# Kernel optimization log

Measured on AMD Instinct MI355X. Metric: run time of the kernel, lower is better.

Reference implementation:

```python
import jax, jax.numpy as jnp
import numpy as np

K = 3  # spatial kernel size (TVConv_k_square == 9)


def setup_inputs() -> dict:
    key = jax.random.key(0)
    k1, k2 = jax.random.split(key)
    B, C, H, W = 8, 96, 128, 128
    x = jax.random.normal(k1, (B, C, H, W), dtype=jnp.float32)
    weight_maps = jax.random.normal(k2, (1, C, K, K, H, W), dtype=jnp.float32)
    return {"x": x, "weight_maps": weight_maps}


def reference(x, weight_maps):
    # Per-pixel spatially-varying 3x3 depthwise conv.
    B, C, H, W = x.shape
    xp = jnp.pad(x, ((0, 0), (0, 0), (1, 1), (1, 1)))  # zero pad, (B,C,H+2,W+2)
    # Gather the 9 shifted views (equivalent to the as_strided unfold, stride 1).
    patches = jnp.stack(
        [xp[:, :, i:i + H, j:j + W] for i in range(K) for j in range(K)], axis=2
    ).reshape(B, C, K, K, H, W)
    # Weighted sum over the 3x3 window per channel per pixel.
    out = (weight_maps * patches).sum(axis=(2, 3))  # (B,C,H,W)
    return out
```

## Files before the change

### kernel.cpp

```cpp
#include <hip/hip_runtime.h>


namespace {
constexpr int B = 8, C = 96, H = 128, W = 128;
constexpr int HW = H * W;
}

__global__ __launch_bounds__(256, 6) void tvconv_kernel(
    const float* __restrict__ x,
    const float* __restrict__ wm,
    float* __restrict__ out) {
  const int t  = threadIdx.x;
  const int c  = blockIdx.x >> 4;
  const int h0 = (blockIdx.x & 15) * 8;
  const int lr = t >> 5;
  const int w4 = t & 31;
  const int h  = h0 + lr;
  const int w  = w4 * 4;

  const float4 zero4 = make_float4(0.f, 0.f, 0.f, 0.f);

  const float* wp = wm + (size_t)c * 9 * HW + h * W + w;
  float4 wt[9];
#pragma unroll
  for (int k = 0; k < 9; ++k) {
    wt[k] = *reinterpret_cast<const float4*>(wp + (size_t)k * HW);
  }

  if (h == 0)     { wt[0] = zero4; wt[1] = zero4; wt[2] = zero4; }
  if (h == H - 1) { wt[6] = zero4; wt[7] = zero4; wt[8] = zero4; }
  const int up = (h == 0)     ? 0 : W;
  const int dn = (h == H - 1) ? 0 : W;

  const bool at_left  = (w4 == 0);
  const bool at_right = (w4 == 31);

  const float* xb = x   + (size_t)c * HW + h * W + w;
  float*       ob = out + (size_t)c * HW + h * W + w;

#pragma unroll
  for (int b = 0; b < B; ++b) {
    const float4 r0 = *reinterpret_cast<const float4*>(xb - up);
    const float4 r1 = *reinterpret_cast<const float4*>(xb);
    const float4 r2 = *reinterpret_cast<const float4*>(xb + dn);
    const float4 rows[3] = {r0, r1, r2};

    float acc[4] = {0.f, 0.f, 0.f, 0.f};
#pragma unroll
    for (int i = 0; i < 3; ++i) {
      const float4 ctr = rows[i];
      float left  = __shfl_up(ctr.w, 1);
      float right = __shfl_down(ctr.x, 1);
      if (at_left)  left  = 0.f;
      if (at_right) right = 0.f;
      const float xv[6] = {left, ctr.x, ctr.y, ctr.z, ctr.w, right};
#pragma unroll
      for (int j = 0; j < 3; ++j) {
        const float4 wv = wt[i * 3 + j];
        const float wa[4] = {wv.x, wv.y, wv.z, wv.w};
#pragma unroll
        for (int m = 0; m < 4; ++m) {
          acc[m] += wa[m] * xv[m + j];
        }
      }
    }
    float4 o;
    o.x = acc[0]; o.y = acc[1]; o.z = acc[2]; o.w = acc[3];
    *reinterpret_cast<float4*>(ob) = o;

    xb += (size_t)C * HW;
    ob += (size_t)C * HW;
  }
}

extern "C" void kernel_launch(void* const* d_in, const int* in_sizes, int n_in,
                              void* d_out, int out_size, void* d_ws, size_t ws_size,
                              hipStream_t stream) {
  const float* x  = (const float*)d_in[0];
  const float* wm = (const float*)d_in[1];
  float* out = (float*)d_out;

  const int blocks = C * (H / 8);
  tvconv_kernel<<<blocks, 256, 0, stream>>>(x, wm, out);
}
```

Measured before the change: 140.9 us.

## Share row loads across wave halves via cross-lane shuffle, prefetch next batch, nontemporal I/O

Each thread now loads only its own row and one neighbour row, and gets the third row from the partner half-wave with __shfl_xor(…,32), cutting input loads per batch from three to two. Loads for the next batch are issued before the current one is computed, to hide memory latency. Weight-map loads and output stores use nontemporal hints to keep them out of the cache. The trade-off is extra shuffles, more live registers, and the possibility that the nontemporal hints lower cache reuse of the weights.

```diff
diff --git a/kernel.cpp b/kernel.cpp
--- a/kernel.cpp
+++ b/kernel.cpp
@@ -5,6 +5,8 @@
 constexpr int B = 8, C = 96, H = 128, W = 128;
 constexpr int HW = H * W;
 }
+
+typedef float f4 __attribute__((ext_vector_type(4)));
 
 __global__ __launch_bounds__(256, 6) void tvconv_kernel(
     const float* __restrict__ x,
@@ -18,19 +20,21 @@
   const int h  = h0 + lr;
   const int w  = w4 * 4;
 
-  const float4 zero4 = make_float4(0.f, 0.f, 0.f, 0.f);
-
   const float* wp = wm + (size_t)c * 9 * HW + h * W + w;
-  float4 wt[9];
+  f4 wt[9];
 #pragma unroll
   for (int k = 0; k < 9; ++k) {
-    wt[k] = *reinterpret_cast<const float4*>(wp + (size_t)k * HW);
+    wt[k] = __builtin_nontemporal_load(
+        reinterpret_cast<const f4*>(wp + (size_t)k * HW));
   }
 
-  if (h == 0)     { wt[0] = zero4; wt[1] = zero4; wt[2] = zero4; }
-  if (h == H - 1) { wt[6] = zero4; wt[7] = zero4; wt[8] = zero4; }
+  if (h == 0)     { wt[0] = 0.f; wt[1] = 0.f; wt[2] = 0.f; }
+  if (h == H - 1) { wt[6] = 0.f; wt[7] = 0.f; wt[8] = 0.f; }
   const int up = (h == 0)     ? 0 : W;
   const int dn = (h == H - 1) ? 0 : W;
+
+  const bool lower = ((lr & 1) == 0);
+  const int ooff = lower ? -up : dn;
 
   const bool at_left  = (w4 == 0);
   const bool at_right = (w4 == 31);
@@ -38,17 +42,34 @@
   const float* xb = x   + (size_t)c * HW + h * W + w;
   float*       ob = out + (size_t)c * HW + h * W + w;
 
+  f4 nctr = *reinterpret_cast<const f4*>(xb);
+  f4 noth = *reinterpret_cast<const f4*>(xb + ooff);
+
 #pragma unroll
   for (int b = 0; b < B; ++b) {
-    const float4 r0 = *reinterpret_cast<const float4*>(xb - up);
-    const float4 r1 = *reinterpret_cast<const float4*>(xb);
-    const float4 r2 = *reinterpret_cast<const float4*>(xb + dn);
-    const float4 rows[3] = {r0, r1, r2};
+    const f4 cc = nctr;
+    const f4 oo = noth;
+    if (b + 1 < B) {
+      xb += (size_t)C * HW;
+      nctr = *reinterpret_cast<const f4*>(xb);
+      noth = *reinterpret_cast<const f4*>(xb + ooff);
+    }
+
+    f4 prt;
+    prt.x = __shfl_xor(cc.x, 32);
+    prt.y = __shfl_xor(cc.y, 32);
+    prt.z = __shfl_xor(cc.z, 32);
+    prt.w = __shfl_xor(cc.w, 32);
+
+    const f4 r0 = lower ? oo  : prt;
+    const f4 r1 = cc;
+    const f4 r2 = lower ? prt : oo;
+    const f4 rows[3] = {r0, r1, r2};
 
     float acc[4] = {0.f, 0.f, 0.f, 0.f};
 #pragma unroll
     for (int i = 0; i < 3; ++i) {
-      const float4 ctr = rows[i];
+      const f4 ctr = rows[i];
       float left  = __shfl_up(ctr.w, 1);
       float right = __shfl_down(ctr.x, 1);
       if (at_left)  left  = 0.f;
@@ -56,7 +77,7 @@
       const float xv[6] = {left, ctr.x, ctr.y, ctr.z, ctr.w, right};
 #pragma unroll
       for (int j = 0; j < 3; ++j) {
-        const float4 wv = wt[i * 3 + j];
+        const f4 wv = wt[i * 3 + j];
         const float wa[4] = {wv.x, wv.y, wv.z, wv.w};
 #pragma unroll
         for (int m = 0; m < 4; ++m) {
@@ -64,11 +85,9 @@
         }
       }
     }
-    float4 o;
+    f4 o;
     o.x = acc[0]; o.y = acc[1]; o.z = acc[2]; o.w = acc[3];
-    *reinterpret_cast<float4*>(ob) = o;
-
-    xb += (size_t)C * HW;
+    __builtin_nontemporal_store(o, reinterpret_cast<f4*>(ob));
     ob += (size_t)C * HW;
   }
 }
```

Measured after the change: 139.5 us. No clear change (-1.0%).

## Compute two output rows per thread, sharing neighbor rows via cross-half shuffle

Applied to the files above, without the earlier changes.

Each thread now produces two adjacent output rows, loading three input rows and getting the fourth from the paired half-wavefront through a shuffle. This cuts redundant x row loads per output. It also prefetches the next batch's rows while computing the current batch, and uses nontemporal loads for weights and nontemporal stores for outputs. Register use roughly doubles (launch bounds lowered to 3 waves), grid size halves, and the boundary and kernel-index remapping logic becomes more intricate.

```diff
diff --git a/kernel.cpp b/kernel.cpp
--- a/kernel.cpp
+++ b/kernel.cpp
@@ -6,70 +6,111 @@
 constexpr int HW = H * W;
 }
 
-__global__ __launch_bounds__(256, 6) void tvconv_kernel(
+typedef float f4 __attribute__((ext_vector_type(4)));
+
+__global__ __launch_bounds__(256, 3) void tvconv_kernel(
     const float* __restrict__ x,
     const float* __restrict__ wm,
     float* __restrict__ out) {
   const int t  = threadIdx.x;
-  const int c  = blockIdx.x >> 4;
-  const int h0 = (blockIdx.x & 15) * 8;
-  const int lr = t >> 5;
+  const int c  = blockIdx.x >> 3;
+  const int h0 = (blockIdx.x & 7) * 16;
+  const int tr = t >> 5;
   const int w4 = t & 31;
-  const int h  = h0 + lr;
   const int w  = w4 * 4;
+  const int h  = h0 + tr * 2;
+  const bool lower = ((tr & 1) == 0);
 
-  const float4 zero4 = make_float4(0.f, 0.f, 0.f, 0.f);
+  const int hP = lower ? h : h + 1;
+  const int hQ = lower ? h + 1 : h;
 
-  const float* wp = wm + (size_t)c * 9 * HW + h * W + w;
-  float4 wt[9];
+  f4 wtP[9], wtQ[9];
+  {
+    const float* wc = wm + (size_t)c * 9 * HW + w;
 #pragma unroll
-  for (int k = 0; k < 9; ++k) {
-    wt[k] = *reinterpret_cast<const float4*>(wp + (size_t)k * HW);
+    for (int k = 0; k < 9; ++k) {
+      const int ti = k / 3, tj = k % 3;
+      const int kk = lower ? k : (6 - 3 * ti + tj);
+      wtP[k] = __builtin_nontemporal_load(
+          reinterpret_cast<const f4*>(wc + (size_t)kk * HW + hP * W));
+      wtQ[k] = __builtin_nontemporal_load(
+          reinterpret_cast<const f4*>(wc + (size_t)kk * HW + hQ * W));
+    }
   }
+  if (hP == 0 || hP == H - 1) { wtP[0] = 0.f; wtP[1] = 0.f; wtP[2] = 0.f; }
 
-  if (h == 0)     { wt[0] = zero4; wt[1] = zero4; wt[2] = zero4; }
-  if (h == H - 1) { wt[6] = zero4; wt[7] = zero4; wt[8] = zero4; }
-  const int up = (h == 0)     ? 0 : W;
-  const int dn = (h == H - 1) ? 0 : W;
+  const int offF = lower ? ((h == 0) ? 0 : -W)
+                         : ((h == H - 2) ? W : 2 * W);
+  const int offM = lower ? 0 : W;
+  const int offN = lower ? W : 0;
 
   const bool at_left  = (w4 == 0);
   const bool at_right = (w4 == 31);
 
-  const float* xb = x   + (size_t)c * HW + h * W + w;
-  float*       ob = out + (size_t)c * HW + h * W + w;
+  const float* xb = x + (size_t)c * HW + h * W + w;
+  float* obP = out + (size_t)c * HW + hP * W + w;
+  float* obQ = out + (size_t)c * HW + hQ * W + w;
+
+  f4 nF = *reinterpret_cast<const f4*>(xb + offF);
+  f4 nM = *reinterpret_cast<const f4*>(xb + offM);
+  f4 nN = *reinterpret_cast<const f4*>(xb + offN);
+
+  auto make_xv = [&](float* xv, const f4 r) {
+    float left  = __shfl_up(r.w, 1);
+    float right = __shfl_down(r.x, 1);
+    if (at_left)  left  = 0.f;
+    if (at_right) right = 0.f;
+    xv[0] = left; xv[1] = r.x; xv[2] = r.y; xv[3] = r.z; xv[4] = r.w;
+    xv[5] = right;
+  };
+  auto acc_row = [&](float* acc, const f4* wt, const int i, const float* xv) {
+#pragma unroll
+    for (int j = 0; j < 3; ++j) {
+      const f4 wv = wt[i * 3 + j];
+      const float wa[4] = {wv.x, wv.y, wv.z, wv.w};
+#pragma unroll
+      for (int m = 0; m < 4; ++m) acc[m] += wa[m] * xv[m + j];
+    }
+  };
 
 #pragma unroll
   for (int b = 0; b < B; ++b) {
-    const float4 r0 = *reinterpret_cast<const float4*>(xb - up);
-    const float4 r1 = *reinterpret_cast<const float4*>(xb);
-    const float4 r2 = *reinterpret_cast<const float4*>(xb + dn);
-    const float4 rows[3] = {r0, r1, r2};
+    const f4 Lf = nF, Lm = nM, Ln = nN;
+    if (b + 1 < B) {
+      xb += (size_t)C * HW;
+      nF = *reinterpret_cast<const f4*>(xb + offF);
+      nM = *reinterpret_cast<const f4*>(xb + offM);
+      nN = *reinterpret_cast<const f4*>(xb + offN);
+    }
 
-    float acc[4] = {0.f, 0.f, 0.f, 0.f};
-#pragma unroll
-    for (int i = 0; i < 3; ++i) {
-      const float4 ctr = rows[i];
-      float left  = __shfl_up(ctr.w, 1);
-      float right = __shfl_down(ctr.x, 1);
-      if (at_left)  left  = 0.f;
-      if (at_right) right = 0.f;
-      const float xv[6] = {left, ctr.x, ctr.y, ctr.z, ctr.w, right};
-#pragma unroll
-      for (int j = 0; j < 3; ++j) {
-        const float4 wv = wt[i * 3 + j];
-        const float wa[4] = {wv.x, wv.y, wv.z, wv.w};
-#pragma unroll
-        for (int m = 0; m < 4; ++m) {
-          acc[m] += wa[m] * xv[m + j];
-        }
-      }
-    }
-    float4 o;
-    o.x = acc[0]; o.y = acc[1]; o.z = acc[2]; o.w = acc[3];
-    *reinterpret_cast<float4*>(ob) = o;
+    f4 P;
+    P.x = __shfl_xor(Ln.x, 32);
+    P.y = __shfl_xor(Ln.y, 32);
+    P.z = __shfl_xor(Ln.z, 32);
+    P.w = __shfl_xor(Ln.w, 32);
 
-    xb += (size_t)C * HW;
-    ob += (size_t)C * HW;
+    float xvF[6], xvM[6], xvN[6], xvP[6];
+    make_xv(xvF, Lf);
+    make_xv(xvM, Lm);
+    make_xv(xvN, Ln);
+    make_xv(xvP, P);
+
+    float accP[4] = {0.f, 0.f, 0.f, 0.f};
+    float accQ[4] = {0.f, 0.f, 0.f, 0.f};
+    acc_row(accP, wtP, 0, xvF);
+    acc_row(accP, wtP, 1, xvM);
+    acc_row(accP, wtP, 2, xvN);
+    acc_row(accQ, wtQ, 0, xvM);
+    acc_row(accQ, wtQ, 1, xvN);
+    acc_row(accQ, wtQ, 2, xvP);
+
+    f4 oP, oQ;
+    oP.x = accP[0]; oP.y = accP[1]; oP.z = accP[2]; oP.w = accP[3];
+    oQ.x = accQ[0]; oQ.y = accQ[1]; oQ.z = accQ[2]; oQ.w = accQ[3];
+    __builtin_nontemporal_store(oP, reinterpret_cast<f4*>(obP));
+    __builtin_nontemporal_store(oQ, reinterpret_cast<f4*>(obQ));
+    obP += (size_t)C * HW;
+    obQ += (size_t)C * HW;
   }
 }
 
@@ -80,6 +121,6 @@
   const float* wm = (const float*)d_in[1];
   float* out = (float*)d_out;
 
-  const int blocks = C * (H / 8);
+  const int blocks = C * (H / 16);
   tvconv_kernel<<<blocks, 256, 0, stream>>>(x, wm, out);
 }
```

New measurement: 138.2 us. About the same (-1.9%).
